# Kernel tuning notes

Hardware: AMD Instinct MI355X
Metric: run time of the kernel (lower is better)

The kernel has to match this reference:

```python
import jax, jax.numpy as jnp
import numpy as np
from jax import lax

B, C, H, W, D = 2, 64, 32, 32, 32
N = H * W * D          # input_size = 32768
P = 64                 # proj_size
NH = 4                 # num_heads
HD = C // NH           # head dim = 16
LN_EPS = 1e-5
BN_EPS = 1e-5


def setup_inputs() -> dict:
    key = jax.random.key(0)
    ks = jax.random.split(key, 10)
    s = lambda k, shape: (jax.random.normal(k, shape, jnp.float32) * 0.02)
    return dict(
        x=jax.random.normal(ks[0], (B, C, H, W, D), jnp.float32),
        ln_w=jnp.ones((C,), jnp.float32), ln_b=jnp.zeros((C,), jnp.float32),
        gamma=1e-6 * jnp.ones((C,), jnp.float32),
        temp1=jnp.ones((NH, 1, 1), jnp.float32),
        temp2=jnp.ones((NH, 1, 1), jnp.float32),
        W_qkvv=s(ks[1], (4 * C, C)),                      # Linear(C,4C), no bias
        W_EF=s(ks[2], (P, N)), b_EF=jnp.zeros((P,), jnp.float32),  # shared E=F
        W_o1=s(ks[3], (C // 2, C)), b_o1=jnp.zeros((C // 2,), jnp.float32),
        W_o2=s(ks[4], (C // 2, C)), b_o2=jnp.zeros((C // 2,), jnp.float32),
        conv1_w=s(ks[5], (C, C, 3, 3, 3)),
        conv2_w=s(ks[6], (C, C, 3, 3, 3)),
        bn1_w=jnp.ones((C,), jnp.float32), bn1_b=jnp.zeros((C,), jnp.float32),
        bn2_w=jnp.ones((C,), jnp.float32), bn2_b=jnp.zeros((C,), jnp.float32),
        conv8_w=s(ks[7], (C, C, 1, 1, 1)), conv8_b=jnp.zeros((C,), jnp.float32),
    )


def _ln(x, w, b):
    mu = jnp.mean(x, axis=-1, keepdims=True)
    var = jnp.mean(jnp.square(x - mu), axis=-1, keepdims=True)
    return (x - mu) * lax.rsqrt(var + LN_EPS) * w + b


def _l2norm(x):  # F.normalize(dim=-1), eps=1e-12
    n = jnp.sqrt(jnp.sum(jnp.square(x), axis=-1, keepdims=True))
    return x / jnp.maximum(n, 1e-12)


def _bn_eval(x, w, b):  # BatchNorm3d in eval mode, running mean 0 / var 1
    scale = (w * lax.rsqrt(jnp.float32(1.0 + BN_EPS))).reshape(1, -1, 1, 1, 1)
    return x * scale + b.reshape(1, -1, 1, 1, 1)


def _conv3d(x, w, pad):
    return lax.conv_general_dilated(
        x, w, window_strides=(1, 1, 1), padding=[(pad, pad)] * 3,
        dimension_numbers=('NCDHW', 'OIDHW', 'NCDHW'))


def _lrelu(x):
    return jnp.where(x >= 0, x, 0.01 * x)


def _epa(xn, W_qkvv, W_EF, b_EF, temp1, temp2, W_o1, b_o1, W_o2, b_o2):
    b, n, c = xn.shape
    qkvv = (xn @ W_qkvv.T).reshape(b, n, 4, NH, HD).transpose(2, 0, 3, 1, 4)  # [4,B,h,N,d]
    q, k, v_ca, v_sa = [jnp.swapaxes(qkvv[i], -2, -1) for i in range(4)]      # [B,h,d,N]
    # shared linear projection E = F over the token axis N -> P
    k_proj = jnp.einsum('bhdn,pn->bhdp', k, W_EF) + b_EF
    v_proj = jnp.einsum('bhdn,pn->bhdp', v_sa, W_EF) + b_EF
    qn, kn = _l2norm(q), _l2norm(k)
    # channel attention: [B,h,d,d]
    attn_ca = jax.nn.softmax(jnp.einsum('bhdn,bhen->bhde', qn, kn) * temp1, axis=-1)
    x_ca = jnp.einsum('bhde,bhen->bhdn', attn_ca, v_ca)                       # [B,h,d,N]
    x_ca = x_ca.transpose(0, 3, 1, 2).reshape(b, n, c)
    # spatial attention with projected K/V: [B,h,N,P]
    attn_sa = jax.nn.softmax(jnp.einsum('bhdn,bhdp->bhnp', qn, k_proj) * temp2, axis=-1)
    x_sa = jnp.einsum('bhnp,bhdp->bhnd', attn_sa, v_proj)                     # [B,h,N,d]
    # faithful to original UNETR++ code: permute(0,3,1,2) then reshape(B,N,C)
    x_sa = x_sa.transpose(0, 3, 1, 2).reshape(b, n, c)
    x_sa = x_sa @ W_o1.T + b_o1
    x_ca = x_ca @ W_o2.T + b_o2
    return jnp.concatenate([x_sa, x_ca], axis=-1)


def reference(x, ln_w, ln_b, gamma, temp1, temp2, W_qkvv, W_EF, b_EF,
              W_o1, b_o1, W_o2, b_o2, conv1_w, conv2_w,
              bn1_w, bn1_b, bn2_w, bn2_b, conv8_w, conv8_b):
    b, c, h, w, d = x.shape
    xs = x.reshape(b, c, h * w * d).transpose(0, 2, 1)  # [B,N,C]
    attn = xs + gamma * _epa(_ln(xs, ln_w, ln_b), W_qkvv, W_EF, b_EF,
                             temp1, temp2, W_o1, b_o1, W_o2, b_o2)
    attn_skip = attn.reshape(b, h, w, d, c).transpose(0, 4, 1, 2, 3)  # [B,C,H,W,D]
    # UnetResBlock (stride 1, in==out -> identity residual), BN in eval mode
    out = _lrelu(_bn_eval(_conv3d(attn_skip, conv1_w, 1), bn1_w, bn1_b))
    out = _bn_eval(_conv3d(out, conv2_w, 1), bn2_w, bn2_b)
    out = _lrelu(out + attn_skip)
    # conv8: Dropout3d (off, eval) + 1x1x1 conv with bias
    y = _conv3d(out, conv8_w, 0) + conv8_b.reshape(1, -1, 1, 1, 1)
    return attn_skip + y
```

## Files before the change

### kernel.cpp

```cpp
#include <hip/hip_runtime.h>

#define NTOK 32768

typedef __attribute__((ext_vector_type(8))) short short8;
typedef __attribute__((ext_vector_type(4))) short short4_t;
typedef __attribute__((ext_vector_type(4))) float f32x4;

__device__ __forceinline__ short f2b(float f) {
    union { float f; unsigned u; } v; v.f = f;
    unsigned r = v.u + 0x7fffu + ((v.u >> 16) & 1u);
    return (short)(r >> 16);
}
__device__ __forceinline__ float b2f(short s) {
    union { float f; unsigned u; } v;
    v.u = ((unsigned)(unsigned short)s) << 16;
    return v.f;
}

__global__ void k_repack(const float* __restrict__ w1, const float* __restrict__ w2,
                         const float* __restrict__ w8, const float* __restrict__ wef,
                         const float* __restrict__ wq, const float* __restrict__ bEF,
                         short* __restrict__ wb1, short* __restrict__ wb2,
                         short* __restrict__ wb8, short* __restrict__ wefb,
                         short* __restrict__ wqb, float* __restrict__ kp,
                         float* __restrict__ vp, float* __restrict__ qd)
{
    int i = blockIdx.x * 256 + threadIdx.x;
    if (i >= 2349312) return;
    if (i >= 2347008) { qd[i - 2347008] = 0.f; return; }
    if (i >= 2338816) {
        int j = i - 2338816;
        float v = bEF[j & 63];
        kp[j] = v; vp[j] = v; return;
    }
    if (i >= 2322432) { int j = i - 2322432; wqb[j] = f2b(wq[j]); return; }
    if (i >= 225280)  { int j = i - 225280;  wefb[j] = f2b(wef[j]); return; }
    if (i >= 221184)  { int j = i - 221184;  wb8[j] = f2b(w8[j]); return; }
    int sel = i >= 110592;
    int j = sel ? i - 110592 : i;
    int tap = j >> 12;
    int r = j & 4095;
    int oc = r >> 6, ic = r & 63;
    const float* w = sel ? w2 : w1;
    short* o = sel ? wb2 : wb1;
    o[j] = f2b(w[(oc * 64 + ic) * 27 + tap]);
}

__global__ __launch_bounds__(256) void k_ln_qkvv(
    const float* __restrict__ x, const float* __restrict__ lnw,
    const float* __restrict__ lnb, const short* __restrict__ wqb,
    short* __restrict__ qkvvb)
{
    __shared__ __align__(16) short Wl[256 * 72];
    __shared__ __align__(16) short tr[256 * 72];
    __shared__ float red1[4][64], red2[4][64];
    __shared__ float mu_s[64], rs_s[64];
    short* al = tr;

    int bid = blockIdx.x;
    int b = bid >> 9;
    int n0 = (bid & 511) << 6;
    int tid = threadIdx.x;

    for (int i = tid; i < 2048; i += 256) {
        int out = i >> 3, q8 = (i & 7) * 8;
        *(short8*)&Wl[out * 72 + q8] = *(const short8*)&wqb[out * 64 + q8];
    }

    int t = tid & 63, cq = tid >> 6;
    float xr[16];
    float s1 = 0.f, s2 = 0.f;
    const float* xb = x + (((size_t)(b * 64 + cq * 16)) << 15) + n0 + t;
#pragma unroll
    for (int j = 0; j < 16; ++j) {
        float v = xb[(size_t)j << 15];
        xr[j] = v; s1 += v; s2 += v * v;
    }
    red1[cq][t] = s1; red2[cq][t] = s2;
    __syncthreads();
    if (tid < 64) {
        float a = red1[0][tid] + red1[1][tid] + red1[2][tid] + red1[3][tid];
        float q = red2[0][tid] + red2[1][tid] + red2[2][tid] + red2[3][tid];
        float mu = a * (1.f / 64.f);
        float var = q * (1.f / 64.f) - mu * mu;
        mu_s[tid] = mu;
        rs_s[tid] = rsqrtf(var + 1e-5f);
    }
    __syncthreads();
    {
        float mu = mu_s[t], rs = rs_s[t];
        short8 p0, p1;
#pragma unroll
        for (int j = 0; j < 8; ++j) {
            int c = cq * 16 + j;
            p0[j] = f2b((xr[j] - mu) * rs * lnw[c] + lnb[c]);
        }
#pragma unroll
        for (int j = 0; j < 8; ++j) {
            int c = cq * 16 + 8 + j;
            p1[j] = f2b((xr[8 + j] - mu) * rs * lnw[c] + lnb[c]);
        }
        *(short8*)&al[t * 72 + cq * 16] = p0;
        *(short8*)&al[t * 72 + cq * 16 + 8] = p1;
    }
    __syncthreads();

    int w = tid >> 6, lane = tid & 63, l15 = lane & 15, quad = lane >> 4;
    f32x4 acc[4][4];
#pragma unroll
    for (int mt = 0; mt < 4; ++mt)
#pragma unroll
        for (int nt = 0; nt < 4; ++nt) acc[mt][nt] = (f32x4){0.f, 0.f, 0.f, 0.f};
#pragma unroll
    for (int ks = 0; ks < 2; ++ks) {
        short8 af[4], bf[4];
#pragma unroll
        for (int mt = 0; mt < 4; ++mt)
            af[mt] = *(const short8*)&al[(mt * 16 + l15) * 72 + quad * 8 + ks * 32];
#pragma unroll
        for (int nt = 0; nt < 4; ++nt)
            bf[nt] = *(const short8*)&Wl[(w * 64 + nt * 16 + l15) * 72 + quad * 8 + ks * 32];
#pragma unroll
        for (int mt = 0; mt < 4; ++mt)
#pragma unroll
            for (int nt = 0; nt < 4; ++nt)
                acc[mt][nt] = __builtin_amdgcn_mfma_f32_16x16x32_bf16(af[mt], bf[nt], acc[mt][nt], 0, 0, 0);
    }
    __syncthreads();

#pragma unroll
    for (int mt = 0; mt < 4; ++mt)
#pragma unroll
        for (int nt = 0; nt < 4; ++nt) {
            int out = w * 64 + nt * 16 + l15;
            short4_t sv;
#pragma unroll
            for (int r = 0; r < 4; ++r) sv[r] = f2b(acc[mt][nt][r]);
            *(short4_t*)&tr[out * 72 + mt * 16 + quad * 4] = sv;
        }
    __syncthreads();
    for (int i = tid; i < 2048; i += 256) {
        int o = i >> 3, tq = (i & 7) * 8;
        short8 v = *(const short8*)&tr[o * 72 + tq];
        int isel = o >> 6, h = (o >> 4) & 3, d = o & 15;
        *(short8*)&qkvvb[((size_t)(((isel * 2 + b) * 4 + h) * 16 + d) << 15) + n0 + tq] = v;
    }
}

__global__ __launch_bounds__(256) void k_pq(
    const short* __restrict__ qkvvb, const short* __restrict__ wefb,
    float* __restrict__ kp, float* __restrict__ vp, float* __restrict__ qd,
    float* __restrict__ qn_acc, float* __restrict__ kn_acc)
{
    __shared__ float redb[3][64][38];
    int kc = blockIdx.x, bh = blockIdx.y;
    int tid = threadIdx.x;
    int w = tid >> 6, lane = tid & 63, l15 = lane & 15, quad = lane >> 4;
    size_t qrow = ((size_t)(bh * 16 + l15)) << 15;
    size_t krow = ((size_t)(128 + bh * 16 + l15)) << 15;
    size_t vrow = ((size_t)(384 + bh * 16 + l15)) << 15;
    int nbase = kc * 1024 + w * 256 + quad * 8;
    f32x4 acck[4], accv[4], accqd, accqq, acckk;
#pragma unroll
    for (int nt = 0; nt < 4; ++nt) {
        acck[nt] = (f32x4){0.f, 0.f, 0.f, 0.f};
        accv[nt] = (f32x4){0.f, 0.f, 0.f, 0.f};
    }
    accqd = (f32x4){0.f, 0.f, 0.f, 0.f};
    accqq = (f32x4){0.f, 0.f, 0.f, 0.f};
    acckk = (f32x4){0.f, 0.f, 0.f, 0.f};
#pragma unroll
    for (int ks = 0; ks < 8; ++ks) {
        int n = nbase + ks * 32;
        short8 qf = *(const short8*)&qkvvb[qrow + n];
        short8 kf = *(const short8*)&qkvvb[krow + n];
        short8 vf = *(const short8*)&qkvvb[vrow + n];
        accqd = __builtin_amdgcn_mfma_f32_16x16x32_bf16(qf, kf, accqd, 0, 0, 0);
        accqq = __builtin_amdgcn_mfma_f32_16x16x32_bf16(qf, qf, accqq, 0, 0, 0);
        acckk = __builtin_amdgcn_mfma_f32_16x16x32_bf16(kf, kf, acckk, 0, 0, 0);
#pragma unroll
        for (int nt = 0; nt < 4; ++nt) {
            short8 wf = *(const short8*)&wefb[(((size_t)(nt * 16 + l15)) << 15) + n];
            acck[nt] = __builtin_amdgcn_mfma_f32_16x16x32_bf16(kf, wf, acck[nt], 0, 0, 0);
            accv[nt] = __builtin_amdgcn_mfma_f32_16x16x32_bf16(vf, wf, accv[nt], 0, 0, 0);
        }
    }
    int diag = (quad == (l15 >> 2));
    float qqv = diag ? accqq[l15 & 3] : 0.f;
    float kkv = diag ? acckk[l15 & 3] : 0.f;
    if (w > 0) {
        float* p = &redb[w - 1][lane][0];
#pragma unroll
        for (int nt = 0; nt < 4; ++nt)
#pragma unroll
            for (int r = 0; r < 4; ++r) { p[nt * 4 + r] = acck[nt][r]; p[16 + nt * 4 + r] = accv[nt][r]; }
#pragma unroll
        for (int r = 0; r < 4; ++r) p[32 + r] = accqd[r];
        p[36] = qqv; p[37] = kkv;
    }
    __syncthreads();
    if (w == 0) {
#pragma unroll
        for (int wv = 0; wv < 3; ++wv) {
            const float* p = &redb[wv][lane][0];
#pragma unroll
            for (int nt = 0; nt < 4; ++nt)
#pragma unroll
                for (int r = 0; r < 4; ++r) { acck[nt][r] += p[nt * 4 + r]; accv[nt][r] += p[16 + nt * 4 + r]; }
#pragma unroll
            for (int r = 0; r < 4; ++r) accqd[r] += p[32 + r];
            qqv += p[36]; kkv += p[37];
        }
        int d = quad * 4;
#pragma unroll
        for (int nt = 0; nt < 4; ++nt)
#pragma unroll
            for (int r = 0; r < 4; ++r) {
                int idx = (bh * 16 + d + r) * 64 + nt * 16 + l15;
                atomicAdd(&kp[idx], acck[nt][r]);
                atomicAdd(&vp[idx], accv[nt][r]);
            }
#pragma unroll
        for (int r = 0; r < 4; ++r)
            atomicAdd(&qd[bh * 256 + (d + r) * 16 + l15], accqd[r]);
        if (diag) {
            atomicAdd(&qn_acc[bh * 16 + l15], qqv);
            atomicAdd(&kn_acc[bh * 16 + l15], kkv);
        }
    }
}

__global__ __launch_bounds__(256) void k_attn(
    const short* __restrict__ qkvvb, const float* __restrict__ qd,
    const float* __restrict__ qn_acc, const float* __restrict__ kn_acc,
    const float* __restrict__ temp1, const float* __restrict__ kp,
    const float* __restrict__ vp, const float* __restrict__ temp2,
    short* __restrict__ xsab, short* __restrict__ xcab)
{
    __shared__ __align__(16) short klT[64 * 24];
    __shared__ __align__(16) short vlb[16 * 72];
    __shared__ __align__(16) short alcab[16 * 24];
    __shared__ float iqs[16], iks[16];
    __shared__ __align__(16) short Pl[4][16][72];
    __shared__ short Ol[4][64][17];
    int bh = blockIdx.y; int b = bh >> 2, h = bh & 3;
    int tid = threadIdx.x;
    if (tid < 32) {
        int j = tid & 15;
        float v = (tid < 16) ? qn_acc[bh * 16 + j] : kn_acc[bh * 16 + j];
        float rv = 1.f / fmaxf(sqrtf(v), 1e-12f);
        if (tid < 16) iqs[j] = rv; else iks[j] = rv;
    }
    __syncthreads();
    for (int i = tid; i < 1024; i += 256) {
        int d = i >> 6, p = i & 63;
        klT[p * 24 + d] = f2b(kp[bh * 1024 + i] * iqs[d]);
        vlb[d * 72 + p] = f2b(vp[bh * 1024 + i]);
    }
    {
        int r = tid >> 4, e = tid & 15;
        float v = qd[bh * 256 + tid] * iqs[r] * iks[e] * temp1[h];
        float mx = v;
#pragma unroll
        for (int m = 1; m < 16; m <<= 1) mx = fmaxf(mx, __shfl_xor(mx, m));
        float ex = __expf(v - mx);
        float s = ex;
#pragma unroll
        for (int m = 1; m < 16; m <<= 1) s += __shfl_xor(s, m);
        alcab[r * 24 + e] = f2b(ex / s);
    }
    __syncthreads();

    int w = tid >> 6, lane = tid & 63, l15 = lane & 15, quad = lane >> 4;
    int tw = (blockIdx.x << 8) + w * 64;
    float t2 = temp2[h];
    const short8 zero8 = {0, 0, 0, 0, 0, 0, 0, 0};
    int xs = (l15 & 7) << 3;

    short8 qb[4];
    if (quad < 2) {
#pragma unroll
        for (int tnt = 0; tnt < 4; ++tnt) {
            short8 v;
#pragma unroll
            for (int j = 0; j < 8; ++j) {
                int d = quad * 8 + j;
                v[j] = qkvvb[(((size_t)(bh * 16 + d)) << 15) + tw + tnt * 16 + l15];
            }
            qb[tnt] = v;
        }
    } else {
#pragma unroll
        for (int tnt = 0; tnt < 4; ++tnt) qb[tnt] = zero8;
    }
    short8 ka[4];
    if (quad < 2) {
#pragma unroll
        for (int pmt = 0; pmt < 4; ++pmt)
            ka[pmt] = *(const short8*)&klT[(pmt * 16 + l15) * 24 + quad * 8];
    } else {
#pragma unroll
        for (int pmt = 0; pmt < 4; ++pmt) ka[pmt] = zero8;
    }

    f32x4 st[4][4];
#pragma unroll
    for (int pmt = 0; pmt < 4; ++pmt)
#pragma unroll
        for (int tnt = 0; tnt < 4; ++tnt) st[pmt][tnt] = (f32x4){0.f, 0.f, 0.f, 0.f};
#pragma unroll
    for (int pmt = 0; pmt < 4; ++pmt)
#pragma unroll
        for (int tnt = 0; tnt < 4; ++tnt)
            st[pmt][tnt] = __builtin_amdgcn_mfma_f32_16x16x32_bf16(ka[pmt], qb[tnt], st[pmt][tnt], 0, 0, 0);

    short8 vb[2];
#pragma unroll
    for (int ks = 0; ks < 2; ++ks)
        vb[ks] = *(const short8*)&vlb[l15 * 72 + quad * 8 + ks * 32];

    f32x4 vo[4];
#pragma unroll
    for (int tnt = 0; tnt < 4; ++tnt) {
        float v[16];
        float mx = -1e30f;
#pragma unroll
        for (int pmt = 0; pmt < 4; ++pmt)
#pragma unroll
            for (int r = 0; r < 4; ++r) {
                float x = st[pmt][tnt][r] * t2;
                v[pmt * 4 + r] = x; mx = fmaxf(mx, x);
            }
        mx = fmaxf(mx, __shfl_xor(mx, 16));
        mx = fmaxf(mx, __shfl_xor(mx, 32));
        float s = 0.f;
#pragma unroll
        for (int i2 = 0; i2 < 16; ++i2) { v[i2] = __expf(v[i2] - mx); s += v[i2]; }
        s += __shfl_xor(s, 16);
        s += __shfl_xor(s, 32);
        float inv = 1.f / s;
#pragma unroll
        for (int pmt = 0; pmt < 4; ++pmt)
#pragma unroll
            for (int t = 0; t < 2; ++t) {
                unsigned lo = (unsigned short)f2b(v[pmt * 4 + 2 * t] * inv);
                unsigned hi = (unsigned short)f2b(v[pmt * 4 + 2 * t + 1] * inv);
                int col = (pmt * 16 + quad * 4 + 2 * t) ^ xs;
                *(unsigned*)&Pl[w][l15][col] = lo | (hi << 16);
            }
        vo[tnt] = (f32x4){0.f, 0.f, 0.f, 0.f};
#pragma unroll
        for (int ks = 0; ks < 2; ++ks) {
            short8 pa = *(const short8*)&Pl[w][l15][(quad * 8 + ks * 32) ^ xs];
            vo[tnt] = __builtin_amdgcn_mfma_f32_16x16x32_bf16(pa, vb[ks], vo[tnt], 0, 0, 0);
        }
    }

    short8 ab[4], bb;
    if (quad < 2) {
        bb = *(const short8*)&alcab[l15 * 24 + quad * 8];
#pragma unroll
        for (int mt = 0; mt < 4; ++mt) {
            short8 u;
#pragma unroll
            for (int j = 0; j < 8; ++j)
                u[j] = qkvvb[(((size_t)(256 + bh * 16 + quad * 8 + j)) << 15) + tw + mt * 16 + l15];
            ab[mt] = u;
        }
    } else {
        bb = zero8;
#pragma unroll
        for (int mt = 0; mt < 4; ++mt) ab[mt] = zero8;
    }
    f32x4 ca[4];
#pragma unroll
    for (int mt = 0; mt < 4; ++mt) ca[mt] = (f32x4){0.f, 0.f, 0.f, 0.f};
#pragma unroll
    for (int mt = 0; mt < 4; ++mt)
        ca[mt] = __builtin_amdgcn_mfma_f32_16x16x32_bf16(ab[mt], bb, ca[mt], 0, 0, 0);

#pragma unroll
    for (int mt = 0; mt < 4; ++mt)
#pragma unroll
        for (int r = 0; r < 4; ++r) {
            int tok = tw + mt * 16 + quad * 4 + r;
            xcab[((size_t)(b * NTOK + tok)) * 64 + h * 16 + l15] = f2b(ca[mt][r]);
        }

#pragma unroll
    for (int mt = 0; mt < 4; ++mt)
#pragma unroll
        for (int r = 0; r < 4; ++r)
            Ol[w][mt * 16 + quad * 4 + r][l15] = f2b(vo[mt][r]);
#pragma unroll
    for (int d = 0; d < 16; ++d) {
        short vv = Ol[w][lane][d];
        xsab[(size_t)b * 2097152 + (((size_t)(d * 4 + h)) << 15) + tw + lane] = vv;
    }
}

__global__ __launch_bounds__(256) void k_epilogue(
    const float* __restrict__ x, const short* __restrict__ xsab,
    const short* __restrict__ xcab, const float* __restrict__ Wo1,
    const float* __restrict__ bo1, const float* __restrict__ Wo2,
    const float* __restrict__ bo2, const float* __restrict__ gamma,
    float* __restrict__ attn_skip, short* __restrict__ gA)
{
    __shared__ __align__(16) short Wl[64 * 72];
    __shared__ __align__(16) short trS[256 * 72];
    int tid = threadIdx.x;
    int bidx = blockIdx.x;
    int b = bidx >> 7;
    int n0 = (bidx & 127) << 8;
    for (int i = tid; i < 4096; i += 256) {
        int row = i >> 6, c = i & 63;
        float wv = (row < 32) ? Wo1[row * 64 + c] : Wo2[(row - 32) * 64 + c];
        Wl[row * 72 + c] = f2b(wv);
    }
    __syncthreads();

    int w = tid >> 6, lane = tid & 63, l15 = lane & 15, quad = lane >> 4;
    int tw = n0 + w * 64;
    const short* sa_base = xsab + (size_t)b * 2097152;
    const short* ca_base = xcab + (size_t)b * 2097152;

    f32x4 acc_sa[4][2], acc_ca[4][2];
#pragma unroll
    for (int mt = 0; mt < 4; ++mt)
#pragma unroll
        for (int nt = 0; nt < 2; ++nt) {
            acc_sa[mt][nt] = (f32x4){0.f, 0.f, 0.f, 0.f};
            acc_ca[mt][nt] = (f32x4){0.f, 0.f, 0.f, 0.f};
        }
#pragma unroll
    for (int ks = 0; ks < 2; ++ks) {
        int ko = quad * 8 + ks * 32;
        short8 b1[2], b2[2];
#pragma unroll
        for (int nt = 0; nt < 2; ++nt) {
            b1[nt] = *(const short8*)&Wl[(nt * 16 + l15) * 72 + ko];
            b2[nt] = *(const short8*)&Wl[(32 + nt * 16 + l15) * 72 + ko];
        }
#pragma unroll
        for (int mt = 0; mt < 4; ++mt) {
            int trow = tw + mt * 16 + l15;
            short8 a1 = *(const short8*)&sa_base[(size_t)trow * 64 + ko];
            short8 a2 = *(const short8*)&ca_base[(size_t)trow * 64 + ko];
#pragma unroll
            for (int nt = 0; nt < 2; ++nt) {
                acc_sa[mt][nt] = __builtin_amdgcn_mfma_f32_16x16x32_bf16(a1, b1[nt], acc_sa[mt][nt], 0, 0, 0);
                acc_ca[mt][nt] = __builtin_amdgcn_mfma_f32_16x16x32_bf16(a2, b2[nt], acc_ca[mt][nt], 0, 0, 0);
            }
        }
    }

#pragma unroll
    for (int half = 0; half < 2; ++half) {
#pragma unroll
        for (int nt = 0; nt < 2; ++nt) {
            int c = half * 32 + nt * 16 + l15;
            float g = gamma[c];
            float bias = half ? bo2[c - 32] : bo1[c];
#pragma unroll
            for (int mt = 0; mt < 4; ++mt) {
                f32x4 a = half ? acc_ca[mt][nt] : acc_sa[mt][nt];
                int tbase = tw + mt * 16 + quad * 4;
                size_t gidx = (((size_t)(b * 64 + c)) << 15) + tbase;
                f32x4 xv = *(const f32x4*)&x[gidx];
                f32x4 o;
#pragma unroll
                for (int r = 0; r < 4; ++r) {
                    float v = xv[r] + g * (a[r] + bias);
                    o[r] = v;
                    trS[(w * 64 + mt * 16 + quad * 4 + r) * 72 + c] = f2b(v);
                }
                *(f32x4*)&attn_skip[gidx] = o;
            }
        }
    }
    __syncthreads();
    for (int i = tid; i < 2048; i += 256) {
        int tok = i >> 3, cq = (i & 7) * 8;
        short8 v = *(const short8*)&trS[tok * 72 + cq];
        *(short8*)&gA[((size_t)(b * NTOK + n0 + tok)) * 64 + cq] = v;
    }
}

template <int MODE>
__global__ __launch_bounds__(256) void k_conv3m(
    const short* __restrict__ gin, const short* __restrict__ wb,
    const float* __restrict__ bnw, const float* __restrict__ bnb,
    const float* __restrict__ skip, short* __restrict__ goutS,
    const short* __restrict__ wb8, const float* __restrict__ b8,
    float* __restrict__ io)
{
    __shared__ __align__(16) short inl_s[24480];
    __shared__ __align__(16) short wl_s[15360];
    int bx = blockIdx.x;
    int bb = bx >> 8;
    int z0 = (bx >> 3) & 31;
    int y0 = (bx & 7) * 4;
    int tid = threadIdx.x;
    int lane = tid & 63, wv = tid >> 6;
    int l15 = lane & 15, quad = lane >> 4;
    int wo = tid >> 2, wq = tid & 3;

    f32x4 acc[2][4];
#pragma unroll
    for (int s = 0; s < 2; ++s)
#pragma unroll
        for (int nt = 0; nt < 4; ++nt) acc[s][nt] = (f32x4){0.f, 0.f, 0.f, 0.f};

    for (int chunk = 0; chunk < 2; ++chunk) {
        const short* wck = wb + chunk * 32 + wq * 8;
        short8 wr[2][3];
#pragma unroll
        for (int t = 0; t < 3; ++t) {
            wr[0][t] = *(const short8*)&wck[(size_t)(t * 64 + wo) * 64];
            wr[1][t] = *(const short8*)&wck[(size_t)((3 + t) * 64 + wo) * 64];
        }
        __syncthreads();
        for (int i = tid; i < 2448; i += 256) {
            int p = i >> 2, icq = i & 3;
            int xi = p % 34; int t2 = p / 34; int yi = t2 % 6; int zi = t2 / 6;
            int gz = z0 + zi - 1, gy = y0 + yi - 1, gx = xi - 1;
            short8 v = {0, 0, 0, 0, 0, 0, 0, 0};
            if ((unsigned)gz < 32u && (unsigned)gy < 32u && (unsigned)gx < 32u)
                v = *(const short8*)&gin[((size_t)(bb * NTOK + gz * 1024 + gy * 32 + gx)) * 64 + chunk * 32 + icq * 8];
            *(short8*)&inl_s[p * 40 + icq * 8] = v;
        }
#pragma unroll
        for (int t = 0; t < 3; ++t)
            *(short8*)&wl_s[(t * 64 + wo) * 40 + wq * 8] = wr[0][t];

#pragma unroll
        for (int kz = 0; kz < 3; ++kz)
#pragma unroll
        for (int ky = 0; ky < 3; ++ky) {
            const int sidx = kz * 3 + ky;
            __syncthreads();
            if (sidx < 7) {
#pragma unroll
                for (int t = 0; t < 3; ++t)
                    wr[sidx & 1][t] = *(const short8*)&wck[(size_t)(((sidx + 2) * 3 + t) * 64 + wo) * 64];
            }
            const short* wcur = &wl_s[(sidx & 1) * 7680];
            int rowb = (kz * 6 + wv + ky) * 34;
#pragma unroll
            for (int kx = 0; kx < 3; ++kx) {
                short8 bf[4];
#pragma unroll
                for (int nt = 0; nt < 4; ++nt)
                    bf[nt] = *(const short8*)&wcur[(kx * 64 + nt * 16 + l15) * 40 + quad * 8];
#pragma unroll
                for (int s = 0; s < 2; ++s) {
                    short8 af = *(const short8*)&inl_s[(rowb + s * 16 + l15 + kx) * 40 + quad * 8];
#pragma unroll
                    for (int nt = 0; nt < 4; ++nt)
                        acc[s][nt] = __builtin_amdgcn_mfma_f32_16x16x32_bf16(af, bf[nt], acc[s][nt], 0, 0, 0);
                }
            }
            if (sidx < 8) {
                short* wnext = &wl_s[((sidx + 1) & 1) * 7680];
#pragma unroll
                for (int t = 0; t < 3; ++t)
                    *(short8*)&wnext[(t * 64 + wo) * 40 + wq * 8] = wr[(sidx + 1) & 1][t];
            }
        }
    }
    __syncthreads();
    float rb = rsqrtf(1.f + 1e-5f);
    if (MODE == 0) {
        short* outS = inl_s;
#pragma unroll
        for (int nt = 0; nt < 4; ++nt) {
            int oc = nt * 16 + l15;
            float sc_ = bnw[oc] * rb, sh_ = bnb[oc];
#pragma unroll
            for (int s = 0; s < 2; ++s) {
                f32x4 v = acc[s][nt];
#pragma unroll
                for (int r = 0; r < 4; ++r) {
                    int pos = wv * 32 + s * 16 + quad * 4 + r;
                    float val = v[r] * sc_ + sh_;
                    val = val >= 0.f ? val : 0.01f * val;
                    outS[pos * 72 + oc] = f2b(val);
                }
            }
        }
        __syncthreads();
        for (int i = tid; i < 1024; i += 256) {
            int p = i >> 3, cq = i & 7;
            short8 v = *(const short8*)&outS[p * 72 + cq * 8];
            int y = p >> 5, x = p & 31;
            *(short8*)&goutS[((size_t)(bb * NTOK + z0 * 1024 + (y0 + y) * 32 + x)) * 64 + cq * 8] = v;
        }
    } else {
        short* a2_s = wl_s;
        short* w8_s = wl_s + 9216;
        f32x4 skr[2][4];
#pragma unroll
        for (int nt = 0; nt < 4; ++nt) {
            int oc = nt * 16 + l15;
            float sc_ = bnw[oc] * rb, sh_ = bnb[oc];
#pragma unroll
            for (int s = 0; s < 2; ++s) {
                size_t g = (((size_t)(bb * 64 + oc)) << 15) +
                           ((z0 * 32 + y0 + wv) * 32 + s * 16 + quad * 4);
                f32x4 sk = *(const f32x4*)&skip[g];
                skr[s][nt] = sk;
                f32x4 v = acc[s][nt];
#pragma unroll
                for (int r = 0; r < 4; ++r) {
                    int pos = wv * 32 + s * 16 + quad * 4 + r;
                    float val = v[r] * sc_ + sh_ + sk[r];
                    val = val >= 0.f ? val : 0.01f * val;
                    a2_s[pos * 72 + oc] = f2b(val);
                }
            }
        }
        for (int i = tid; i < 512; i += 256) {
            int ocw = i >> 3, cq = i & 7;
            *(short8*)&w8_s[ocw * 80 + cq * 8] = *(const short8*)&wb8[ocw * 64 + cq * 8];
        }
        __syncthreads();
        f32x4 acc2[2][4];
#pragma unroll
        for (int s = 0; s < 2; ++s)
#pragma unroll
            for (int nt = 0; nt < 4; ++nt) acc2[s][nt] = (f32x4){0.f, 0.f, 0.f, 0.f};
#pragma unroll
        for (int ks = 0; ks < 2; ++ks) {
            short8 a8[2], b8f[4];
#pragma unroll
            for (int s = 0; s < 2; ++s)
                a8[s] = *(const short8*)&a2_s[(wv * 32 + s * 16 + l15) * 72 + quad * 8 + ks * 32];
#pragma unroll
            for (int nt = 0; nt < 4; ++nt)
                b8f[nt] = *(const short8*)&w8_s[(nt * 16 + l15) * 80 + quad * 8 + ks * 32];
#pragma unroll
            for (int s = 0; s < 2; ++s)
#pragma unroll
                for (int nt = 0; nt < 4; ++nt)
                    acc2[s][nt] = __builtin_amdgcn_mfma_f32_16x16x32_bf16(a8[s], b8f[nt], acc2[s][nt], 0, 0, 0);
        }
#pragma unroll
        for (int nt = 0; nt < 4; ++nt) {
            int oc = nt * 16 + l15;
            float bias8 = b8[oc];
#pragma unroll
            for (int s = 0; s < 2; ++s) {
                size_t g = (((size_t)(bb * 64 + oc)) << 15) +
                           ((z0 * 32 + y0 + wv) * 32 + s * 16 + quad * 4);
                f32x4 o;
#pragma unroll
                for (int r = 0; r < 4; ++r) o[r] = skr[s][nt][r] + acc2[s][nt][r] + bias8;
                *(f32x4*)&io[g] = o;
            }
        }
    }
}

extern "C" void kernel_launch(void* const* d_in, const int* in_sizes, int n_in,
                              void* d_out, int out_size, void* d_ws, size_t ws_size,
                              hipStream_t stream) {
    const float* x      = (const float*)d_in[0];
    const float* ln_w   = (const float*)d_in[1];
    const float* ln_b   = (const float*)d_in[2];
    const float* gamma  = (const float*)d_in[3];
    const float* temp1  = (const float*)d_in[4];
    const float* temp2  = (const float*)d_in[5];
    const float* W_qkvv = (const float*)d_in[6];
    const float* W_EF   = (const float*)d_in[7];
    const float* b_EF   = (const float*)d_in[8];
    const float* W_o1   = (const float*)d_in[9];
    const float* b_o1   = (const float*)d_in[10];
    const float* W_o2   = (const float*)d_in[11];
    const float* b_o2   = (const float*)d_in[12];
    const float* conv1w = (const float*)d_in[13];
    const float* conv2w = (const float*)d_in[14];
    const float* bn1_w  = (const float*)d_in[15];
    const float* bn1_b  = (const float*)d_in[16];
    const float* bn2_w  = (const float*)d_in[17];
    const float* bn2_b  = (const float*)d_in[18];
    const float* conv8w = (const float*)d_in[19];
    const float* conv8b = (const float*)d_in[20];

    short* qkvvb = (short*)d_ws;
    float* kp    = (float*)(qkvvb + 16777216);
    float* vp    = kp + 8192;
    float* qd    = vp + 8192;
    float* qn_acc= qd + 2048;
    float* kn_acc= qn_acc + 128;
    float* a_ca  = kn_acc + 128;
    float* iqn   = a_ca + 2048;
    float* ikn   = iqn + 128;
    short* xcab  = (short*)(ikn + 128);
    short* xsab  = xcab + 4194304;
    short* gA    = xsab + 4194304;
    short* g1    = gA + 4194304;
    short* wb1   = g1 + 4194304;
    short* wb2   = wb1 + 110592;
    short* wb8   = wb2 + 110592;
    short* wefb  = wb8 + 4096;
    short* wqb   = wefb + 2097152;

    float* attn_skip = (float*)d_out;

    hipLaunchKernelGGL(k_repack, dim3(9177), dim3(256), 0, stream,
                       conv1w, conv2w, conv8w, W_EF, W_qkvv, b_EF,
                       wb1, wb2, wb8, wefb, wqb, kp, vp, qd);
    hipLaunchKernelGGL(k_ln_qkvv, dim3(1024), dim3(256), 0, stream,
                       x, ln_w, ln_b, wqb, qkvvb);
    hipLaunchKernelGGL(k_pq, dim3(32, 8), dim3(256), 0, stream,
                       qkvvb, wefb, kp, vp, qd, qn_acc, kn_acc);
    hipLaunchKernelGGL(k_attn, dim3(128, 8), dim3(256), 0, stream,
                       qkvvb, qd, qn_acc, kn_acc, temp1, kp, vp, temp2, xsab, xcab);
    hipLaunchKernelGGL(k_epilogue, dim3(256), dim3(256), 0, stream,
                       x, xsab, xcab, W_o1, b_o1, W_o2, b_o2, gamma, attn_skip, gA);
    hipLaunchKernelGGL((k_conv3m<0>), dim3(512), dim3(256), 0, stream,
                       gA, wb1, bn1_w, bn1_b, (const float*)nullptr, g1,
                       (const short*)nullptr, (const float*)nullptr, (float*)nullptr);
    hipLaunchKernelGGL((k_conv3m<1>), dim3(512), dim3(256), 0, stream,
                       g1, wb2, bn2_w, bn2_b, attn_skip, (short*)nullptr,
                       wb8, conv8b, attn_skip);
}
```

Baseline: 209.9 us.

## Halve conv3d block tile to two rows and stage weights per tap

The implicit-GEMM 3x3x3 conv kernels now give each block a 2-row tile (64 voxels) instead of 4 rows, and launch twice as many blocks. Weight staging moves from one (kz,ky) row of three taps to a single tap per double-buffered stage, which shrinks LDS use from about 80KB to about 38KB per block so more blocks can sit on each CU. In exchange there are 27 barriers per chunk instead of 9, only 4 MFMAs run between barriers, and the input halo is re-read more often relative to useful output.

```diff
diff --git a/kernel.cpp b/kernel.cpp
--- a/kernel.cpp
+++ b/kernel.cpp
@@ -494,78 +494,56 @@
     const short* __restrict__ wb8, const float* __restrict__ b8,
     float* __restrict__ io)
 {
-    __shared__ __align__(16) short inl_s[24480];
-    __shared__ __align__(16) short wl_s[15360];
+    __shared__ __align__(16) short inl_s[14688];
+    __shared__ __align__(16) short wl_s[4608];
     int bx = blockIdx.x;
-    int bb = bx >> 8;
-    int z0 = (bx >> 3) & 31;
-    int y0 = (bx & 7) * 4;
+    int bb = bx >> 9;
+    int z0 = (bx >> 4) & 31;
+    int y0 = (bx & 15) * 2;
     int tid = threadIdx.x;
     int lane = tid & 63, wv = tid >> 6;
     int l15 = lane & 15, quad = lane >> 4;
     int wo = tid >> 2, wq = tid & 3;
-
-    f32x4 acc[2][4];
-#pragma unroll
-    for (int s = 0; s < 2; ++s)
-#pragma unroll
-        for (int nt = 0; nt < 4; ++nt) acc[s][nt] = (f32x4){0.f, 0.f, 0.f, 0.f};
+    int yloc = wv >> 1, sx = wv & 1;
+    int pbase = yloc * 32 + sx * 16;
+
+    f32x4 acc[4];
+#pragma unroll
+    for (int nt = 0; nt < 4; ++nt) acc[nt] = (f32x4){0.f, 0.f, 0.f, 0.f};
 
     for (int chunk = 0; chunk < 2; ++chunk) {
         const short* wck = wb + chunk * 32 + wq * 8;
-        short8 wr[2][3];
-#pragma unroll
-        for (int t = 0; t < 3; ++t) {
-            wr[0][t] = *(const short8*)&wck[(size_t)(t * 64 + wo) * 64];
-            wr[1][t] = *(const short8*)&wck[(size_t)((3 + t) * 64 + wo) * 64];
-        }
+        short8 wr[2];
+        wr[0] = *(const short8*)&wck[(size_t)wo * 64];
+        wr[1] = *(const short8*)&wck[(size_t)(64 + wo) * 64];
         __syncthreads();
-        for (int i = tid; i < 2448; i += 256) {
+        for (int i = tid; i < 1632; i += 256) {
             int p = i >> 2, icq = i & 3;
-            int xi = p % 34; int t2 = p / 34; int yi = t2 % 6; int zi = t2 / 6;
+            int xi = p % 34; int t2 = p / 34; int yi = t2 & 3; int zi = t2 >> 2;
             int gz = z0 + zi - 1, gy = y0 + yi - 1, gx = xi - 1;
             short8 v = {0, 0, 0, 0, 0, 0, 0, 0};
             if ((unsigned)gz < 32u && (unsigned)gy < 32u && (unsigned)gx < 32u)
                 v = *(const short8*)&gin[((size_t)(bb * NTOK + gz * 1024 + gy * 32 + gx)) * 64 + chunk * 32 + icq * 8];
-            *(short8*)&inl_s[p * 40 + icq * 8] = v;
-        }
-#pragma unroll
-        for (int t = 0; t < 3; ++t)
-            *(short8*)&wl_s[(t * 64 + wo) * 40 + wq * 8] = wr[0][t];
-
-#pragma unroll
-        for (int kz = 0; kz < 3; ++kz)
-#pragma unroll
-        for (int ky = 0; ky < 3; ++ky) {
-            const int sidx = kz * 3 + ky;
+            *(short8*)&inl_s[p * 36 + icq * 8] = v;
+        }
+        *(short8*)&wl_s[wo * 36 + wq * 8] = wr[0];
+
+#pragma unroll
+        for (int tap = 0; tap < 27; ++tap) {
             __syncthreads();
-            if (sidx < 7) {
-#pragma unroll
-                for (int t = 0; t < 3; ++t)
-                    wr[sidx & 1][t] = *(const short8*)&wck[(size_t)(((sidx + 2) * 3 + t) * 64 + wo) * 64];
-            }
-            const short* wcur = &wl_s[(sidx & 1) * 7680];
-            int rowb = (kz * 6 + wv + ky) * 34;
-#pragma unroll
-            for (int kx = 0; kx < 3; ++kx) {
-                short8 bf[4];
-#pragma unroll
-                for (int nt = 0; nt < 4; ++nt)
-                    bf[nt] = *(const short8*)&wcur[(kx * 64 + nt * 16 + l15) * 40 + quad * 8];
-#pragma unroll
-                for (int s = 0; s < 2; ++s) {
-                    short8 af = *(const short8*)&inl_s[(rowb + s * 16 + l15 + kx) * 40 + quad * 8];
-#pragma unroll
-                    for (int nt = 0; nt < 4; ++nt)
-                        acc[s][nt] = __builtin_amdgcn_mfma_f32_16x16x32_bf16(af, bf[nt], acc[s][nt], 0, 0, 0);
-                }
-            }
-            if (sidx < 8) {
-                short* wnext = &wl_s[((sidx + 1) & 1) * 7680];
-#pragma unroll
-                for (int t = 0; t < 3; ++t)
-                    *(short8*)&wnext[(t * 64 + wo) * 40 + wq * 8] = wr[(sidx + 1) & 1][t];
-            }
+            if (tap < 25)
+                wr[tap & 1] = *(const short8*)&wck[(size_t)((tap + 2) * 64 + wo) * 64];
+            const short* wcur = &wl_s[(tap & 1) * 2304];
+            int kz = tap / 9, ky = (tap / 3) % 3, kx = tap % 3;
+            int arow = (kz * 4 + yloc + ky) * 34 + sx * 16 + l15 + kx;
+            short8 af = *(const short8*)&inl_s[arow * 36 + quad * 8];
+#pragma unroll
+            for (int nt = 0; nt < 4; ++nt) {
+                short8 bf = *(const short8*)&wcur[(nt * 16 + l15) * 36 + quad * 8];
+                acc[nt] = __builtin_amdgcn_mfma_f32_16x16x32_bf16(af, bf, acc[nt], 0, 0, 0);
+            }
+            if (tap < 26)
+                *(short8*)&wl_s[((tap + 1) & 1) * 2304 + wo * 36 + wq * 8] = wr[(tap + 1) & 1];
         }
     }
     __syncthreads();
@@ -576,47 +554,41 @@
         for (int nt = 0; nt < 4; ++nt) {
             int oc = nt * 16 + l15;
             float sc_ = bnw[oc] * rb, sh_ = bnb[oc];
-#pragma unroll
-            for (int s = 0; s < 2; ++s) {
-                f32x4 v = acc[s][nt];
-#pragma unroll
-                for (int r = 0; r < 4; ++r) {
-                    int pos = wv * 32 + s * 16 + quad * 4 + r;
-                    float val = v[r] * sc_ + sh_;
-                    val = val >= 0.f ? val : 0.01f * val;
-                    outS[pos * 72 + oc] = f2b(val);
-                }
+            f32x4 v = acc[nt];
+#pragma unroll
+            for (int r = 0; r < 4; ++r) {
+                int pos = pbase + quad * 4 + r;
+                float val = v[r] * sc_ + sh_;
+                val = val >= 0.f ? val : 0.01f * val;
+                outS[pos * 72 + oc] = f2b(val);
             }
         }
         __syncthreads();
-        for (int i = tid; i < 1024; i += 256) {
+        for (int i = tid; i < 512; i += 256) {
             int p = i >> 3, cq = i & 7;
             short8 v = *(const short8*)&outS[p * 72 + cq * 8];
             int y = p >> 5, x = p & 31;
             *(short8*)&goutS[((size_t)(bb * NTOK + z0 * 1024 + (y0 + y) * 32 + x)) * 64 + cq * 8] = v;
         }
     } else {
-        short* a2_s = wl_s;
-        short* w8_s = wl_s + 9216;
-        f32x4 skr[2][4];
+        short* a2_s = inl_s;
+        short* w8_s = inl_s + 4608;
+        f32x4 skr[4];
 #pragma unroll
         for (int nt = 0; nt < 4; ++nt) {
             int oc = nt * 16 + l15;
             float sc_ = bnw[oc] * rb, sh_ = bnb[oc];
-#pragma unroll
-            for (int s = 0; s < 2; ++s) {
-                size_t g = (((size_t)(bb * 64 + oc)) << 15) +
-                           ((z0 * 32 + y0 + wv) * 32 + s * 16 + quad * 4);
-                f32x4 sk = *(const f32x4*)&skip[g];
-                skr[s][nt] = sk;
-                f32x4 v = acc[s][nt];
-#pragma unroll
-                for (int r = 0; r < 4; ++r) {
-                    int pos = wv * 32 + s * 16 + quad * 4 + r;
-                    float val = v[r] * sc_ + sh_ + sk[r];
-                    val = val >= 0.f ? val : 0.01f * val;
-                    a2_s[pos * 72 + oc] = f2b(val);
-                }
+            size_t g = (((size_t)(bb * 64 + oc)) << 15) +
+                       ((z0 * 32 + y0 + yloc) * 32 + sx * 16 + quad * 4);
+            f32x4 sk = *(const f32x4*)&skip[g];
+            skr[nt] = sk;
+            f32x4 v = acc[nt];
+#pragma unroll
+            for (int r = 0; r < 4; ++r) {
+                int pos = pbase + quad * 4 + r;
+                float val = v[r] * sc_ + sh_ + sk[r];
+                val = val >= 0.f ? val : 0.01f * val;
+                a2_s[pos * 72 + oc] = f2b(val);
             }
         }
         for (int i = tid; i < 512; i += 256) {
@@ -624,39 +596,28 @@
             *(short8*)&w8_s[ocw * 80 + cq * 8] = *(const short8*)&wb8[ocw * 64 + cq * 8];
         }
         __syncthreads();
-        f32x4 acc2[2][4];
-#pragma unroll
-        for (int s = 0; s < 2; ++s)
-#pragma unroll
-            for (int nt = 0; nt < 4; ++nt) acc2[s][nt] = (f32x4){0.f, 0.f, 0.f, 0.f};
+        f32x4 acc2[4];
+#pragma unroll
+        for (int nt = 0; nt < 4; ++nt) acc2[nt] = (f32x4){0.f, 0.f, 0.f, 0.f};
 #pragma unroll
         for (int ks = 0; ks < 2; ++ks) {
-            short8 a8[2], b8f[4];
-#pragma unroll
-            for (int s = 0; s < 2; ++s)
-                a8[s] = *(const short8*)&a2_s[(wv * 32 + s * 16 + l15) * 72 + quad * 8 + ks * 32];
-#pragma unroll
-            for (int nt = 0; nt < 4; ++nt)
-                b8f[nt] = *(const short8*)&w8_s[(nt * 16 + l15) * 80 + quad * 8 + ks * 32];
-#pragma unroll
-            for (int s = 0; s < 2; ++s)
-#pragma unroll
-                for (int nt = 0; nt < 4; ++nt)
-                    acc2[s][nt] = __builtin_amdgcn_mfma_f32_16x16x32_bf16(a8[s], b8f[nt], acc2[s][nt], 0, 0, 0);
+            short8 a8 = *(const short8*)&a2_s[(pbase + l15) * 72 + quad * 8 + ks * 32];
+#pragma unroll
+            for (int nt = 0; nt < 4; ++nt) {
+                short8 b8f = *(const short8*)&w8_s[(nt * 16 + l15) * 80 + quad * 8 + ks * 32];
+                acc2[nt] = __builtin_amdgcn_mfma_f32_16x16x32_bf16(a8, b8f, acc2[nt], 0, 0, 0);
+            }
         }
 #pragma unroll
         for (int nt = 0; nt < 4; ++nt) {
             int oc = nt * 16 + l15;
             float bias8 = b8[oc];
-#pragma unroll
-            for (int s = 0; s < 2; ++s) {
-                size_t g = (((size_t)(bb * 64 + oc)) << 15) +
-                           ((z0 * 32 + y0 + wv) * 32 + s * 16 + quad * 4);
-                f32x4 o;
-#pragma unroll
-                for (int r = 0; r < 4; ++r) o[r] = skr[s][nt][r] + acc2[s][nt][r] + bias8;
-                *(f32x4*)&io[g] = o;
-            }
+            size_t g = (((size_t)(bb * 64 + oc)) << 15) +
+                       ((z0 * 32 + y0 + yloc) * 32 + sx * 16 + quad * 4);
+            f32x4 o;
+#pragma unroll
+            for (int r = 0; r < 4; ++r) o[r] = skr[nt][r] + acc2[nt][r] + bias8;
+            *(f32x4*)&io[g] = o;
         }
     }
 }
@@ -718,10 +679,10 @@
                        qkvvb, qd, qn_acc, kn_acc, temp1, kp, vp, temp2, xsab, xcab);
     hipLaunchKernelGGL(k_epilogue, dim3(256), dim3(256), 0, stream,
                        x, xsab, xcab, W_o1, b_o1, W_o2, b_o2, gamma, attn_skip, gA);
-    hipLaunchKernelGGL((k_conv3m<0>), dim3(512), dim3(256), 0, stream,
+    hipLaunchKernelGGL((k_conv3m<0>), dim3(1024), dim3(256), 0, stream,
                        gA, wb1, bn1_w, bn1_b, (const float*)nullptr, g1,
                        (const short*)nullptr, (const float*)nullptr, (float*)nullptr);
-    hipLaunchKernelGGL((k_conv3m<1>), dim3(512), dim3(256), 0, stream,
+    hipLaunchKernelGGL((k_conv3m<1>), dim3(1024), dim3(256), 0, stream,
                        g1, wb2, bn2_w, bn2_b, attn_skip, (short*)nullptr,
                        wb8, conv8b, attn_skip);
 }
```

After: 384.3 us. +83.1%, slower.
